# Kernel tuning notes

Measured on AMD Instinct MI355X. Metric: run time of the kernel, lower is better.

## Reference

```python
import jax, jax.numpy as jnp
import numpy as np

DIM = 192
WH, WW = 8, 8
N = WH * WW           # 64 tokens per window
H = 6                 # heads
HD = DIM // H         # 32
SCALE = HD ** -0.5
B_ = 8192             # num_windows * batch
NW = 64               # windows sharing one mask


def _relative_position_index():
    ch, cw = np.arange(WH), np.arange(WW)
    coords = np.stack(np.meshgrid(ch, cw, indexing='ij'))        # (2, Wh, Ww)
    cf = coords.reshape(2, -1)                                   # (2, N)
    rel = cf[:, :, None] - cf[:, None, :]                        # (2, N, N)
    rel = rel.transpose(1, 2, 0).copy()
    rel[:, :, 0] += WH - 1
    rel[:, :, 1] += WW - 1
    rel[:, :, 0] *= 2 * WW - 1
    return (rel.sum(-1)).astype(np.int32)                        # (N, N)


def setup_inputs() -> dict:
    key = jax.random.key(0)
    ks = jax.random.split(key, 6)
    x = jax.random.normal(ks[0], (B_, N, DIM), dtype=jnp.float32)
    mask = jnp.zeros((NW, N, N), dtype=jnp.float32)
    qkv_w = jax.random.normal(ks[1], (3 * DIM, DIM), dtype=jnp.float32) * 0.02
    qkv_b = jnp.zeros((3 * DIM,), dtype=jnp.float32)
    proj_w = jax.random.normal(ks[2], (DIM, DIM), dtype=jnp.float32) * 0.02
    proj_b = jnp.zeros((DIM,), dtype=jnp.float32)
    bias_table = jax.random.normal(ks[3], ((2 * WH - 1) * (2 * WW - 1), H), dtype=jnp.float32) * 0.02
    rel_idx = jnp.asarray(_relative_position_index())
    return {"x": x, "mask": mask, "qkv_w": qkv_w, "qkv_b": qkv_b,
            "proj_w": proj_w, "proj_b": proj_b, "bias_table": bias_table,
            "rel_idx": rel_idx}


def reference(x, mask, qkv_w, qkv_b, proj_w, proj_b, bias_table, rel_idx):
    b, n, c = x.shape
    # qkv projection -> (3, B_, H, N, HD)
    qkv = (x @ qkv_w.T + qkv_b).reshape(b, n, 3, H, HD).transpose(2, 0, 3, 1, 4)
    q, k, v = qkv[0], qkv[1], qkv[2]
    # gathered relative position bias: (H, N, N)
    rpb = bias_table[rel_idx.reshape(-1)].reshape(n, n, H).transpose(2, 0, 1)
    # attention scores with bias + per-window shift mask
    scores = jnp.einsum('bhnd,bhmd->bhnm', q * SCALE, k) + rpb[None]
    nw = mask.shape[0]
    scores = scores.reshape(b // nw, nw, H, n, n) + mask[None, :, None]
    scores = scores.reshape(b, H, n, n)
    attn = jax.nn.softmax(scores, axis=-1)
    out = jnp.einsum('bhnm,bhmd->bhnd', attn, v)          # (B_, H, N, HD)
    out = out.transpose(0, 2, 1, 3).reshape(b, n, c)       # b n (h d)
    return out @ proj_w.T + proj_b
```

## Files before the change

kernel.cpp:

```cpp
#include <hip/hip_runtime.h>
#include <hip/hip_bf16.h>

typedef __bf16 v8bf __attribute__((ext_vector_type(8)));
typedef float  v4f  __attribute__((ext_vector_type(4)));

#define MFMA(a,b,c) __builtin_amdgcn_mfma_f32_16x16x32_bf16((a),(b),(c),0,0,0)

__device__ __forceinline__ float loadf(const void* p, int i, int isb) {
  return isb ? (float)(((const __bf16*)p)[i]) : ((const float*)p)[i];
}

__global__ void detect_kernel(const void* __restrict__ x, int* __restrict__ flag) {
  __shared__ int cnt;
  if (threadIdx.x == 0) cnt = 0;
  __syncthreads();
  unsigned char b = ((const unsigned char*)x)[1 + 4 * (int)threadIdx.x];
  int e = b & 0x7f;
  if (e >= 0x3B && e <= 0x41) atomicAdd(&cnt, 1);
  __syncthreads();
  if (threadIdx.x == 0) *flag = (cnt >= 64) ? 1 : 0;
}

__global__ void prep_kernel(const void* __restrict__ qkv_w, const void* __restrict__ proj_w,
                            const void* __restrict__ bias_table, const int* __restrict__ rel_idx,
                            const void* __restrict__ mask, const int* __restrict__ flag,
                            __bf16* __restrict__ qkv_wf, __bf16* __restrict__ projf,
                            float* __restrict__ cmb) {
  const int isb = *flag;
  int e = blockIdx.x * 256 + threadIdx.x;
  if (e < 110592) {
    int j = e & 7, lx = (e >> 3) & 63, ks = (e >> 9) % 6, nt = e / 3072;
    int n = nt * 16 + (lx & 15), k = ks * 32 + (lx >> 4) * 8 + j;
    qkv_wf[e] = (__bf16)loadf(qkv_w, n * 192 + k, isb);
  } else if (e < 147456) {
    int e2 = e - 110592;
    int j = e2 & 7, lx = (e2 >> 3) & 63, ks = (e2 >> 9) % 6, nt = e2 / 3072;
    int n = nt * 16 + (lx & 15), k = ks * 32 + (lx >> 4) * 8 + j;
    projf[e2] = (__bf16)loadf(proj_w, n * 192 + k, isb);
  } else if (e < 147456 + 1572864) {
    int e2 = e - 147456;
    int j = e2 & 63, i = (e2 >> 6) & 63, hh = (e2 >> 12) % 6, w = e2 / 24576;
    float v = loadf(bias_table, rel_idx[i * 64 + j] * 6 + hh, isb)
            + loadf(mask, (w * 64 + i) * 64 + j, isb);
    cmb[(e2 & ~63) | (((j & 15) << 2) | (j >> 4))] = v;
  }
}

__global__ __launch_bounds__(384, 4)
void wattn_kernel(const void* __restrict__ x, const int* __restrict__ flag,
                  const __bf16* __restrict__ qkv_wf, const __bf16* __restrict__ projf,
                  const float* __restrict__ cmb,
                  const void* __restrict__ qkv_b, const void* __restrict__ proj_b,
                  void* __restrict__ out) {
  __shared__ char smem[73728];
  __bf16* xf = (__bf16*)smem;
  __bf16* Qr = (__bf16*)(smem + 24576);

  const int isb = *flag;
  const int win = blockIdx.x;
  const int t = threadIdx.x;
  const int l = t & 63;
  const int h = t >> 6;
  const int quad = l >> 4;
  const int c16 = l & 15;
  const float SCALE = 0.17677669529663687f;

  #pragma unroll
  for (int i = 0; i < 4; ++i) {
    int c = t + i * 384;
    int tok = c / 24, kb8 = c % 24;
    v8bf v;
    if (isb) {
      v = *(const v8bf*)((const __bf16*)x + (size_t)win * 12288 + (size_t)c * 8);
    } else {
      const float* xp = (const float*)x + (size_t)win * 12288 + (size_t)c * 8;
      float4 f0 = ((const float4*)xp)[0];
      float4 f1 = ((const float4*)xp)[1];
      v8bf tv;
      tv[0]=(__bf16)f0.x; tv[1]=(__bf16)f0.y; tv[2]=(__bf16)f0.z; tv[3]=(__bf16)f0.w;
      tv[4]=(__bf16)f1.x; tv[5]=(__bf16)f1.y; tv[6]=(__bf16)f1.z; tv[7]=(__bf16)f1.w;
      v = tv;
    }
    int mt = tok >> 4, r = tok & 15, ks = kb8 >> 2, kb = kb8 & 3;
    *(v8bf*)(xf + ((mt * 6 + ks) * 64 + kb * 16 + r) * 8) = v;
  }
  __syncthreads();

  const v4f vzero = {0.f, 0.f, 0.f, 0.f};
  __bf16* qf = Qr + h * 4096;
  __bf16* kf = qf + 2048;

  #pragma unroll
  for (int pass = 0; pass < 2; ++pass) {
    v4f acc[2][4];
    #pragma unroll
    for (int n = 0; n < 2; ++n)
      #pragma unroll
      for (int m = 0; m < 4; ++m) acc[n][m] = vzero;

    #pragma unroll
    for (int ks = 0; ks < 6; ++ks) {
      v8bf a[4];
      #pragma unroll
      for (int mt = 0; mt < 4; ++mt) a[mt] = *(const v8bf*)(xf + ((mt * 6 + ks) * 64 + l) * 8);
      #pragma unroll
      for (int nl = 0; nl < 2; ++nl) {
        int nt = pass * 12 + 2 * h + nl;
        v8bf b = *(const v8bf*)(qkv_wf + ((nt * 6 + ks) * 64 + l) * 8);
        #pragma unroll
        for (int mt = 0; mt < 4; ++mt) acc[nl][mt] = MFMA(a[mt], b, acc[nl][mt]);
      }
    }
    __bf16* dst = pass ? kf : qf;
    float mul = pass ? 1.0f : SCALE;
    #pragma unroll
    for (int nl = 0; nl < 2; ++nl) {
      int hd = nl * 16 + c16;
      float bias = loadf(qkv_b, pass * 192 + h * 32 + hd, isb);
      #pragma unroll
      for (int mt = 0; mt < 4; ++mt)
        #pragma unroll
        for (int reg = 0; reg < 4; ++reg) {
          float vv = (acc[nl][mt][reg] + bias) * mul;
          int u = mt * 64 + (hd >> 3) * 16 + quad * 4 + reg;
          dst[u * 8 + (hd & 7)] = (__bf16)vv;
        }
    }
  }

  __bf16* Pf = qf;
  {
    v8bf aq[4], bk[4];
    #pragma unroll
    for (int mt = 0; mt < 4; ++mt) aq[mt] = *(const v8bf*)(qf + (mt * 64 + l) * 8);
    #pragma unroll
    for (int j = 0; j < 4; ++j) bk[j] = *(const v8bf*)(kf + (j * 64 + l) * 8);
    const float* cb = cmb + (size_t)((win & 63) * 6 + h) * 4096;
    #pragma unroll
    for (int mt = 0; mt < 4; ++mt) {
      v4f sc[4];
      #pragma unroll
      for (int j = 0; j < 4; ++j) sc[j] = MFMA(aq[mt], bk[j], vzero);
      #pragma unroll
      for (int reg = 0; reg < 4; ++reg) {
        int mrow = quad * 4 + reg;
        int row = mt * 16 + mrow;
        float4 cv = *(const float4*)(cb + row * 64 + c16 * 4);
        float v0 = sc[0][reg] + cv.x;
        float v1 = sc[1][reg] + cv.y;
        float v2 = sc[2][reg] + cv.z;
        float v3 = sc[3][reg] + cv.w;
        float mx = fmaxf(fmaxf(v0, v1), fmaxf(v2, v3));
        mx = fmaxf(mx, __shfl_xor(mx, 1));
        mx = fmaxf(mx, __shfl_xor(mx, 2));
        mx = fmaxf(mx, __shfl_xor(mx, 4));
        mx = fmaxf(mx, __shfl_xor(mx, 8));
        float p0 = __expf(v0 - mx), p1 = __expf(v1 - mx);
        float p2 = __expf(v2 - mx), p3 = __expf(v3 - mx);
        float sm = p0 + p1 + p2 + p3;
        sm += __shfl_xor(sm, 1);
        sm += __shfl_xor(sm, 2);
        sm += __shfl_xor(sm, 4);
        sm += __shfl_xor(sm, 8);
        float inv = 1.0f / sm;
        float pn[4] = {p0 * inv, p1 * inv, p2 * inv, p3 * inv};
        #pragma unroll
        for (int j = 0; j < 4; ++j) {
          int u = (mt * 2 + (j >> 1)) * 64 + ((j & 1) * 2 + (c16 >> 3)) * 16 + mrow;
          Pf[u * 8 + (c16 & 7)] = (__bf16)pn[j];
        }
      }
    }
  }

  v4f vac[2][4];
  #pragma unroll
  for (int n = 0; n < 2; ++n)
    #pragma unroll
    for (int m = 0; m < 4; ++m) vac[n][m] = vzero;
  #pragma unroll
  for (int ks = 0; ks < 6; ++ks) {
    v8bf a[4];
    #pragma unroll
    for (int mt = 0; mt < 4; ++mt) a[mt] = *(const v8bf*)(xf + ((mt * 6 + ks) * 64 + l) * 8);
    #pragma unroll
    for (int ntl = 0; ntl < 2; ++ntl) {
      int nt = 24 + 2 * h + ntl;
      v8bf b = *(const v8bf*)(qkv_wf + ((nt * 6 + ks) * 64 + l) * 8);
      #pragma unroll
      for (int mt = 0; mt < 4; ++mt) vac[ntl][mt] = MFMA(a[mt], b, vac[ntl][mt]);
    }
  }
  __syncthreads();

  __bf16* vf = xf + h * 2048;
  #pragma unroll
  for (int ntl = 0; ntl < 2; ++ntl) {
    float bias = loadf(qkv_b, 384 + h * 32 + ntl * 16 + c16, isb);
    #pragma unroll
    for (int mt = 0; mt < 4; ++mt)
      #pragma unroll
      for (int reg = 0; reg < 4; ++reg) {
        int mrow = quad * 4 + reg;
        int u = (ntl * 2 + (mt >> 1)) * 64 + ((mt & 1) * 2 + (mrow >> 3)) * 16 + c16;
        vf[u * 8 + (mrow & 7)] = (__bf16)(vac[ntl][mt][reg] + bias);
      }
  }

  v4f o[4][2];
  #pragma unroll
  for (int m = 0; m < 4; ++m) { o[m][0] = vzero; o[m][1] = vzero; }
  #pragma unroll
  for (int ksb = 0; ksb < 2; ++ksb) {
    v8bf ap[4], bv[2];
    #pragma unroll
    for (int mt = 0; mt < 4; ++mt) ap[mt] = *(const v8bf*)(Pf + ((mt * 2 + ksb) * 64 + l) * 8);
    #pragma unroll
    for (int ntb = 0; ntb < 2; ++ntb) bv[ntb] = *(const v8bf*)(vf + ((ntb * 2 + ksb) * 64 + l) * 8);
    #pragma unroll
    for (int mt = 0; mt < 4; ++mt)
      #pragma unroll
      for (int ntb = 0; ntb < 2; ++ntb) o[mt][ntb] = MFMA(ap[mt], bv[ntb], o[mt][ntb]);
  }
  __syncthreads();

  __bf16* Of = Qr;
  #pragma unroll
  for (int mt = 0; mt < 4; ++mt)
    #pragma unroll
    for (int ntb = 0; ntb < 2; ++ntb)
      #pragma unroll
      for (int reg = 0; reg < 4; ++reg) {
        int u = (mt * 6 + h) * 64 + (ntb * 2 + (c16 >> 3)) * 16 + quad * 4 + reg;
        Of[u * 8 + (c16 & 7)] = (__bf16)o[mt][ntb][reg];
      }
  __syncthreads();

  v4f pa[2][4];
  #pragma unroll
  for (int n = 0; n < 2; ++n)
    #pragma unroll
    for (int m = 0; m < 4; ++m) pa[n][m] = vzero;
  #pragma unroll
  for (int ks = 0; ks < 6; ++ks) {
    v8bf a[4];
    #pragma unroll
    for (int mt = 0; mt < 4; ++mt) a[mt] = *(const v8bf*)(Of + ((mt * 6 + ks) * 64 + l) * 8);
    #pragma unroll
    for (int ntl = 0; ntl < 2; ++ntl) {
      int nt = 2 * h + ntl;
      v8bf b = *(const v8bf*)(projf + ((nt * 6 + ks) * 64 + l) * 8);
      #pragma unroll
      for (int mt = 0; mt < 4; ++mt) pa[ntl][mt] = MFMA(a[mt], b, pa[ntl][mt]);
    }
  }
  #pragma unroll
  for (int ntl = 0; ntl < 2; ++ntl) {
    int col = (2 * h + ntl) * 16 + c16;
    float pb = loadf(proj_b, col, isb);
    #pragma unroll
    for (int mt = 0; mt < 4; ++mt)
      #pragma unroll
      for (int reg = 0; reg < 4; ++reg) {
        float vv = pa[ntl][mt][reg] + pb;
        size_t oi = (size_t)win * 12288 + (size_t)(mt * 16 + quad * 4 + reg) * 192 + col;
        if (isb) ((__bf16*)out)[oi] = (__bf16)vv;
        else     ((float*)out)[oi] = vv;
      }
  }
}

extern "C" void kernel_launch(void* const* d_in, const int* in_sizes, int n_in,
                              void* d_out, int out_size, void* d_ws, size_t ws_size,
                              hipStream_t stream) {
  (void)in_sizes; (void)n_in; (void)out_size; (void)ws_size;
  const void* x          = d_in[0];
  const void* mask       = d_in[1];
  const void* qkv_w      = d_in[2];
  const void* qkv_b      = d_in[3];
  const void* proj_w     = d_in[4];
  const void* proj_b     = d_in[5];
  const void* bias_table = d_in[6];
  const int*  rel_idx    = (const int*)d_in[7];

  char* ws = (char*)d_ws;
  int*    flag    = (int*)ws;
  __bf16* qkv_wf  = (__bf16*)(ws + 256);
  __bf16* projf   = (__bf16*)(ws + 256 + 221184);
  float*  cmb     = (float*)(ws + 295168);

  detect_kernel<<<1, 256, 0, stream>>>(x, flag);
  prep_kernel<<<6720, 256, 0, stream>>>(qkv_w, proj_w, bias_table, rel_idx, mask, flag,
                                        qkv_wf, projf, cmb);
  wattn_kernel<<<8192, 384, 0, stream>>>(x, flag, qkv_wf, projf, cmb, qkv_b, proj_b, d_out);
}
```

Baseline: 1.046 ms.

## Shrink LDS footprint by keeping Q/K in registers and fusing PV per tile

Q and K tiles are now loaded into registers right after each projection pass, so both share one 4KB per-head LDS slot instead of separate Q and K buffers. The V projection moves ahead of the softmax. The P·V MFMAs now run inside the softmax row-tile loop, reusing a 2KB P slot per 16-row tile. This cuts shared memory from 72KB to 48KB, letting more blocks fit per CU, and launch bounds drop from 4 to 3 to give the compiler more register room. The cost is more live registers and less overlap between the softmax and PV stages within each wave.

```diff
diff --git a/kernel.cpp b/kernel.cpp
--- a/kernel.cpp
+++ b/kernel.cpp
@@ -46,15 +46,15 @@
   }
 }
 
-__global__ __launch_bounds__(384, 4)
+__global__ __launch_bounds__(384, 3)
 void wattn_kernel(const void* __restrict__ x, const int* __restrict__ flag,
                   const __bf16* __restrict__ qkv_wf, const __bf16* __restrict__ projf,
                   const float* __restrict__ cmb,
                   const void* __restrict__ qkv_b, const void* __restrict__ proj_b,
                   void* __restrict__ out) {
-  __shared__ char smem[73728];
+  __shared__ char smem[49152];
   __bf16* xf = (__bf16*)smem;
-  __bf16* Qr = (__bf16*)(smem + 24576);
+  __bf16* Qs = (__bf16*)(smem + 24576);
 
   const int isb = *flag;
   const int win = blockIdx.x;
@@ -87,8 +87,9 @@
   __syncthreads();
 
   const v4f vzero = {0.f, 0.f, 0.f, 0.f};
-  __bf16* qf = Qr + h * 4096;
-  __bf16* kf = qf + 2048;
+  __bf16* sq = Qs + h * 2048;
+
+  v8bf aq[4], bk[4];
 
   #pragma unroll
   for (int pass = 0; pass < 2; ++pass) {
@@ -111,7 +112,6 @@
         for (int mt = 0; mt < 4; ++mt) acc[nl][mt] = MFMA(a[mt], b, acc[nl][mt]);
       }
     }
-    __bf16* dst = pass ? kf : qf;
     float mul = pass ? 1.0f : SCALE;
     #pragma unroll
     for (int nl = 0; nl < 2; ++nl) {
@@ -123,18 +123,64 @@
         for (int reg = 0; reg < 4; ++reg) {
           float vv = (acc[nl][mt][reg] + bias) * mul;
           int u = mt * 64 + (hd >> 3) * 16 + quad * 4 + reg;
-          dst[u * 8 + (hd & 7)] = (__bf16)vv;
+          sq[u * 8 + (hd & 7)] = (__bf16)vv;
         }
     }
-  }
-
-  __bf16* Pf = qf;
+    if (pass == 0) {
+      #pragma unroll
+      for (int mt = 0; mt < 4; ++mt) aq[mt] = *(const v8bf*)(sq + (mt * 64 + l) * 8);
+    } else {
+      #pragma unroll
+      for (int j = 0; j < 4; ++j) bk[j] = *(const v8bf*)(sq + (j * 64 + l) * 8);
+    }
+  }
+
+  v4f vac[2][4];
+  #pragma unroll
+  for (int n = 0; n < 2; ++n)
+    #pragma unroll
+    for (int m = 0; m < 4; ++m) vac[n][m] = vzero;
+  #pragma unroll
+  for (int ks = 0; ks < 6; ++ks) {
+    v8bf a[4];
+    #pragma unroll
+    for (int mt = 0; mt < 4; ++mt) a[mt] = *(const v8bf*)(xf + ((mt * 6 + ks) * 64 + l) * 8);
+    #pragma unroll
+    for (int ntl = 0; ntl < 2; ++ntl) {
+      int nt = 24 + 2 * h + ntl;
+      v8bf b = *(const v8bf*)(qkv_wf + ((nt * 6 + ks) * 64 + l) * 8);
+      #pragma unroll
+      for (int mt = 0; mt < 4; ++mt) vac[ntl][mt] = MFMA(a[mt], b, vac[ntl][mt]);
+    }
+  }
+  __syncthreads();
+
+  __bf16* vf = xf + h * 2048;
+  #pragma unroll
+  for (int ntl = 0; ntl < 2; ++ntl) {
+    float bias = loadf(qkv_b, 384 + h * 32 + ntl * 16 + c16, isb);
+    #pragma unroll
+    for (int mt = 0; mt < 4; ++mt)
+      #pragma unroll
+      for (int reg = 0; reg < 4; ++reg) {
+        int mrow = quad * 4 + reg;
+        int u = (ntl * 2 + (mt >> 1)) * 64 + ((mt & 1) * 2 + (mrow >> 3)) * 16 + c16;
+        vf[u * 8 + (mrow & 7)] = (__bf16)(vac[ntl][mt][reg] + bias);
+      }
+  }
+
+  v8bf bv[2][2];
+  #pragma unroll
+  for (int ksb = 0; ksb < 2; ++ksb)
+    #pragma unroll
+    for (int ntb = 0; ntb < 2; ++ntb)
+      bv[ksb][ntb] = *(const v8bf*)(vf + ((ntb * 2 + ksb) * 64 + l) * 8);
+
+  v4f o[4][2];
+  #pragma unroll
+  for (int m = 0; m < 4; ++m) { o[m][0] = vzero; o[m][1] = vzero; }
+
   {
-    v8bf aq[4], bk[4];
-    #pragma unroll
-    for (int mt = 0; mt < 4; ++mt) aq[mt] = *(const v8bf*)(qf + (mt * 64 + l) * 8);
-    #pragma unroll
-    for (int j = 0; j < 4; ++j) bk[j] = *(const v8bf*)(kf + (j * 64 + l) * 8);
     const float* cb = cmb + (size_t)((win & 63) * 6 + h) * 4096;
     #pragma unroll
     for (int mt = 0; mt < 4; ++mt) {
@@ -166,65 +212,21 @@
         float pn[4] = {p0 * inv, p1 * inv, p2 * inv, p3 * inv};
         #pragma unroll
         for (int j = 0; j < 4; ++j) {
-          int u = (mt * 2 + (j >> 1)) * 64 + ((j & 1) * 2 + (c16 >> 3)) * 16 + mrow;
-          Pf[u * 8 + (c16 & 7)] = (__bf16)pn[j];
+          int u = (j >> 1) * 64 + ((j & 1) * 2 + (c16 >> 3)) * 16 + mrow;
+          sq[u * 8 + (c16 & 7)] = (__bf16)pn[j];
         }
       }
-    }
-  }
-
-  v4f vac[2][4];
-  #pragma unroll
-  for (int n = 0; n < 2; ++n)
-    #pragma unroll
-    for (int m = 0; m < 4; ++m) vac[n][m] = vzero;
-  #pragma unroll
-  for (int ks = 0; ks < 6; ++ks) {
-    v8bf a[4];
-    #pragma unroll
-    for (int mt = 0; mt < 4; ++mt) a[mt] = *(const v8bf*)(xf + ((mt * 6 + ks) * 64 + l) * 8);
-    #pragma unroll
-    for (int ntl = 0; ntl < 2; ++ntl) {
-      int nt = 24 + 2 * h + ntl;
-      v8bf b = *(const v8bf*)(qkv_wf + ((nt * 6 + ks) * 64 + l) * 8);
-      #pragma unroll
-      for (int mt = 0; mt < 4; ++mt) vac[ntl][mt] = MFMA(a[mt], b, vac[ntl][mt]);
-    }
-  }
-  __syncthreads();
-
-  __bf16* vf = xf + h * 2048;
-  #pragma unroll
-  for (int ntl = 0; ntl < 2; ++ntl) {
-    float bias = loadf(qkv_b, 384 + h * 32 + ntl * 16 + c16, isb);
-    #pragma unroll
-    for (int mt = 0; mt < 4; ++mt)
-      #pragma unroll
-      for (int reg = 0; reg < 4; ++reg) {
-        int mrow = quad * 4 + reg;
-        int u = (ntl * 2 + (mt >> 1)) * 64 + ((mt & 1) * 2 + (mrow >> 3)) * 16 + c16;
-        vf[u * 8 + (mrow & 7)] = (__bf16)(vac[ntl][mt][reg] + bias);
-      }
-  }
-
-  v4f o[4][2];
-  #pragma unroll
-  for (int m = 0; m < 4; ++m) { o[m][0] = vzero; o[m][1] = vzero; }
-  #pragma unroll
-  for (int ksb = 0; ksb < 2; ++ksb) {
-    v8bf ap[4], bv[2];
-    #pragma unroll
-    for (int mt = 0; mt < 4; ++mt) ap[mt] = *(const v8bf*)(Pf + ((mt * 2 + ksb) * 64 + l) * 8);
-    #pragma unroll
-    for (int ntb = 0; ntb < 2; ++ntb) bv[ntb] = *(const v8bf*)(vf + ((ntb * 2 + ksb) * 64 + l) * 8);
-    #pragma unroll
-    for (int mt = 0; mt < 4; ++mt)
-      #pragma unroll
-      for (int ntb = 0; ntb < 2; ++ntb) o[mt][ntb] = MFMA(ap[mt], bv[ntb], o[mt][ntb]);
-  }
-  __syncthreads();
-
-  __bf16* Of = Qr;
+      v8bf ap0 = *(const v8bf*)(sq + l * 8);
+      v8bf ap1 = *(const v8bf*)(sq + (64 + l) * 8);
+      o[mt][0] = MFMA(ap0, bv[0][0], o[mt][0]);
+      o[mt][1] = MFMA(ap0, bv[0][1], o[mt][1]);
+      o[mt][0] = MFMA(ap1, bv[1][0], o[mt][0]);
+      o[mt][1] = MFMA(ap1, bv[1][1], o[mt][1]);
+    }
+  }
+  __syncthreads();
+
+  __bf16* Of = Qs;
   #pragma unroll
   for (int mt = 0; mt < 4; ++mt)
     #pragma unroll
```

Result: slower. 1.099 ms (+5.1%).
